# Kernel optimization log

Hardware: AMD Instinct MI355X
Metric: run time of the kernel (lower is better)

## Reference

```python
import jax, jax.numpy as jnp
import numpy as np

T, H, I, E, K = 1024, 1024, 512, 32, 4   # tokens, hidden, moe_inter, n_experts, top_k
G, TG, NS = 8, 4, 2                      # n_group, topk_group, n_shared_experts
C = 2 * T * K // E                       # expert capacity (no-drop headroom)
SCALE = 2.5                              # routed_scaling_factor


def setup_inputs() -> dict:
    key = jax.random.key(0)
    ks = jax.random.split(key, 7)
    s = 0.02
    return dict(
        hidden_states=jax.random.normal(ks[0], (T, H), jnp.float32),
        gate_w=jax.random.normal(ks[1], (E, H), jnp.float32) * s,
        e_bias=jax.random.normal(ks[2], (E,), jnp.float32) * 0.1,
        w_gate_up=jax.random.normal(ks[3], (E, 2 * I, H), jnp.float32) * s,
        w_down=jax.random.normal(ks[4], (E, H, I), jnp.float32) * s,
        w_gate_up_shared=jax.random.normal(ks[5], (2 * I * NS, H), jnp.float32) * s,
        w_down_shared=jax.random.normal(ks[6], (H, I * NS), jnp.float32) * s,
    )


def reference(hidden_states, gate_w, e_bias, w_gate_up, w_down, w_gate_up_shared, w_down_shared):
    x = hidden_states                                   # (T, H)
    # --- gate + sigmoid scoring (noaux_tc) ---
    logits = x @ gate_w.T                               # (T, E)
    scores = jax.nn.sigmoid(logits.astype(jnp.float32))
    sfc = scores + e_bias                               # scores_for_choice
    # --- group-limited top-k: top-2 sum per group, keep topk_group groups ---
    group_scores = jax.lax.top_k(sfc.reshape(T, G, E // G), 2)[0].sum(-1)  # (T, G)
    grp_idx = jax.lax.top_k(group_scores, TG)[1]        # (T, TG)
    gmask = jnp.zeros((T, G), jnp.float32).at[jnp.arange(T)[:, None], grp_idx].set(1.0)
    smask = jnp.repeat(gmask, E // G, axis=1)           # (T, E)
    sfc_m = jnp.where(smask > 0, sfc, 0.0)
    topk_idx = jax.lax.top_k(sfc_m, K)[1]               # (T, K)
    tw = jnp.take_along_axis(scores, topk_idx, axis=1)  # weights from raw scores
    tw = tw / (tw.sum(-1, keepdims=True) + 1e-20)       # norm_topk_prob
    tw = tw * SCALE
    # --- capacity-based dispatch (position within expert via cumsum of one-hot) ---
    e_flat = topk_idx.reshape(-1)                       # (T*K,)
    oh = jax.nn.one_hot(e_flat, E, dtype=jnp.float32)   # (T*K, E)
    pos = jnp.sum((jnp.cumsum(oh, axis=0) - 1.0) * oh, axis=-1).astype(jnp.int32)
    keep = (pos < C).astype(jnp.float32)                # capacity sized to never drop
    pos_c = jnp.clip(pos, 0, C - 1)
    t_flat = jnp.repeat(jnp.arange(T), K)
    combine = jnp.zeros((T, E, C), jnp.float32).at[t_flat, e_flat, pos_c].add(tw.reshape(-1) * keep)
    dispatch = jnp.zeros((T, E, C), jnp.float32).at[t_flat, e_flat, pos_c].add(keep)
    # --- grouped expert MLP (gate_up -> SiluAndMul -> down) ---
    xe = jnp.einsum('tec,th->ech', dispatch, x)         # (E, C, H)
    gu = jnp.einsum('ech,eoh->eco', xe, w_gate_up)      # (E, C, 2I)
    act = jax.nn.silu(gu[..., :I]) * gu[..., I:]
    ye = jnp.einsum('eci,ehi->ech', act, w_down)        # (E, C, H)
    routed = jnp.einsum('tec,ech->th', combine, ye)     # (T, H)
    # --- shared experts MLP on residual ---
    IS = I * NS
    gus = x @ w_gate_up_shared.T                        # (T, 2*IS)
    acts = jax.nn.silu(gus[:, :IS]) * gus[:, IS:]
    shared = acts @ w_down_shared.T                     # (T, H)
    return routed + shared
```

## Files before the change

kernel.cpp:

```cpp
#include <hip/hip_runtime.h>
#include <hip/hip_bf16.h>
#include <math.h>

#define T_TOK 1024
#define H_DIM 1024
#define I_DIM 512
#define E_NUM 32
#define K_TOP 4
#define G_NUM 8
#define TG_NUM 4
#define CAP 256
#define IS_DIM 1024
#define RSCALE 2.5f

#define MAXTILES 72

#define WS_CNT_OFF    0
#define WS_NT_OFF     128
#define WS_TILE_OFF   256
#define WS_EIDX_OFF   4096
#define WS_WN_OFF     20480
#define WS_STOK_OFF   36864
#define WS_SW_OFF     69632
#define WS_XB_OFF     102400
#define WS_ACT_OFF    (102400 + (size_t)T_TOK*H_DIM*2)
#define WS_ACTS_OFF   (WS_ACT_OFF + (size_t)E_NUM*CAP*I_DIM*2)

typedef __attribute__((ext_vector_type(8))) short short8v;
typedef __attribute__((ext_vector_type(4))) float f32x4;
typedef __attribute__((ext_vector_type(4))) unsigned uint4v;

__device__ __forceinline__ short f2bf(float f) {
    unsigned u = __float_as_uint(f);
    u += 0x7FFFu + ((u >> 16) & 1u);
    return (short)(u >> 16);
}
__device__ __forceinline__ unsigned pk2bf(float a, float b) {
    unsigned ua = __float_as_uint(a) + 0x8000u;
    unsigned ub = __float_as_uint(b) + 0x8000u;
    return __builtin_amdgcn_perm(ub, ua, 0x07060302);
}
__device__ __forceinline__ uint4v pk8bf(float4 lo, float4 hi) {
    uint4v r; r.x = pk2bf(lo.x, lo.y); r.y = pk2bf(lo.z, lo.w);
    r.z = pk2bf(hi.x, hi.y); r.w = pk2bf(hi.z, hi.w); return r;
}
__device__ __forceinline__ float silu_(float g) { return g / (1.f + expf(-g)); }

#define LDSTRIDE 40

__global__ __launch_bounds__(256) void xconv_kernel(const float* __restrict__ x,
                                                    short* __restrict__ xb) {
    const int i = (blockIdx.x * 256 + threadIdx.x) * 8;
    float4 a = *(const float4*)(x + i);
    float4 b = *(const float4*)(x + i + 4);
    *(uint4v*)(xb + i) = pk8bf(a, b);
}

__global__ __launch_bounds__(256) void gate_kernel(
    const float* __restrict__ x, const float* __restrict__ gate_w,
    const float* __restrict__ e_bias,
    int* __restrict__ eidx, float* __restrict__ wnorm)
{
    __shared__ float xs[H_DIM];
    __shared__ float logits[E_NUM];
    const int t = blockIdx.x;
    const int tid = threadIdx.x;
    ((float4*)xs)[tid] = ((const float4*)(x + (size_t)t * H_DIM))[tid];
    __syncthreads();

    const int e = tid >> 3, sub = tid & 7;
    const float4* gw4 = (const float4*)(gate_w + (size_t)e * H_DIM + sub * 128);
    const float4* xr4 = (const float4*)(xs + sub * 128);
    float p = 0.f;
    #pragma unroll
    for (int h = 0; h < 32; ++h) {
        float4 a = xr4[h], b = gw4[h];
        p += a.x * b.x + a.y * b.y + a.z * b.z + a.w * b.w;
    }
    for (int off = 4; off; off >>= 1) p += __shfl_down(p, off, 8);
    if (sub == 0) logits[e] = p;
    __syncthreads();
    if (tid != 0) return;

    float sc[E_NUM], sfc[E_NUM];
    for (int i = 0; i < E_NUM; ++i) {
        sc[i] = 1.f / (1.f + expf(-logits[i]));
        sfc[i] = sc[i] + e_bias[i];
    }
    float gs[G_NUM];
    for (int g = 0; g < G_NUM; ++g) {
        float m1 = -1e30f, m2 = -1e30f;
        for (int j = 0; j < E_NUM / G_NUM; ++j) {
            float v = sfc[g * (E_NUM / G_NUM) + j];
            if (v > m1) { m2 = m1; m1 = v; } else if (v > m2) m2 = v;
        }
        gs[g] = m1 + m2;
    }
    bool gm[G_NUM];
    for (int g = 0; g < G_NUM; ++g) gm[g] = false;
    for (int it = 0; it < TG_NUM; ++it) {
        int best = -1; float bv = -1e30f;
        for (int g = 0; g < G_NUM; ++g) if (!gm[g] && gs[g] > bv) { bv = gs[g]; best = g; }
        gm[best] = true;
    }
    float sm[E_NUM];
    for (int i = 0; i < E_NUM; ++i) sm[i] = gm[i / (E_NUM / G_NUM)] ? sfc[i] : 0.0f;
    int idx[K_TOP]; float w[K_TOP]; float tsum = 0.f;
    for (int it = 0; it < K_TOP; ++it) {
        int best = 0; float bv = -1e30f;
        for (int i = 0; i < E_NUM; ++i) if (sm[i] > bv) { bv = sm[i]; best = i; }
        sm[best] = -1e30f;
        idx[it] = best; w[it] = sc[best]; tsum += w[it];
    }
    float inv = RSCALE / (tsum + 1e-20f);
    const int base = t * K_TOP;
    for (int it = 0; it < K_TOP; ++it) {
        eidx[base + it] = idx[it];
        wnorm[base + it] = w[it] * inv;
    }
}

__global__ __launch_bounds__(256) void assign_kernel(
    const int* __restrict__ eidx, const float* __restrict__ wnorm,
    int* __restrict__ cnt, int* __restrict__ slot_token, float* __restrict__ slot_w,
    int* __restrict__ ntiles, int* __restrict__ tiles)
{
    __shared__ int   se[T_TOK * K_TOP];
    __shared__ float swt[T_TOK * K_TOP];
    __shared__ int   scnt[E_NUM];
    const int tid = threadIdx.x;
    for (int i = tid; i < T_TOK * K_TOP; i += 256) { se[i] = eidx[i]; swt[i] = wnorm[i]; }
    __syncthreads();

    const int e = tid >> 3;
    const int seg = tid & 7;
    const int base = seg * 512;
    int c = 0;
    for (int i = 0; i < 512; ++i) c += (se[base + i] == e);
    int excl = 0, total = 0;
    for (int s = 0; s < 8; ++s) {
        int cs = __shfl(c, s, 8);
        total += cs;
        if (s < seg) excl += cs;
    }
    if (seg == 0) { cnt[e] = total; scnt[e] = total; }
    int pos = excl;
    for (int i = 0; i < 512; ++i) {
        if (se[base + i] == e) {
            if (pos < CAP) {
                slot_token[e * CAP + pos] = (base + i) >> 2;
                slot_w[e * CAP + pos] = swt[base + i];
            }
            ++pos;
        }
    }
    __syncthreads();
    if (tid == 0) {
        int nt = 0;
        for (int t0 = 0; t0 < T_TOK; t0 += 128) {
            tiles[nt * 4] = -1; tiles[nt * 4 + 1] = t0; tiles[nt * 4 + 2] = 128; ++nt;
        }
        for (int ee = 0; ee < E_NUM; ++ee) {
            int n = min(scnt[ee], CAP);
            for (int r = 0; r < n; r += 128) {
                tiles[nt * 4] = ee; tiles[nt * 4 + 1] = r; tiles[nt * 4 + 2] = n; ++nt;
            }
        }
        *ntiles = nt;
    }
}

#define WAVE_SETUP() \
    const int tid = threadIdx.x; const int lane = tid & 63; const int wid = tid >> 6; \
    const int wm = wid & 1, wn = wid >> 1; \
    const int lr16 = lane & 15, kc = lane >> 4; \
    const int srow = tid >> 1, kh = (tid & 1) * 16;

#define DECL_ACC() f32x4 acc[4][4]; \
    _Pragma("unroll") for (int i_ = 0; i_ < 4; ++i_) \
    _Pragma("unroll") for (int j_ = 0; j_ < 4; ++j_) acc[i_][j_] = 0.f;

#define COMPUTE_4x4(Asb, Bsb) do { \
    short8v a_[4], b_[4]; \
    _Pragma("unroll") for (int mt = 0; mt < 4; ++mt) \
        a_[mt] = *(const short8v*)&(Asb)[(wm*64 + mt*16 + lr16)*LDSTRIDE + kc*8]; \
    _Pragma("unroll") for (int nt = 0; nt < 4; ++nt) \
        b_[nt] = *(const short8v*)&(Bsb)[(wn*64 + nt*16 + lr16)*LDSTRIDE + kc*8]; \
    _Pragma("unroll") for (int mt = 0; mt < 4; ++mt) \
    _Pragma("unroll") for (int nt = 0; nt < 4; ++nt) \
        acc[mt][nt] = __builtin_amdgcn_mfma_f32_16x16x32_bf16(a_[mt], b_[nt], acc[mt][nt], 0, 0, 0); \
} while (0)

__global__ __launch_bounds__(256, 3) void gu_all_kernel(
    const short* __restrict__ xb, const float* __restrict__ w_gate_up,
    const float* __restrict__ w_gus,
    const int* __restrict__ ntiles, const int* __restrict__ tiles,
    const int* __restrict__ slot_token, const float* __restrict__ slot_w,
    short* __restrict__ act, short* __restrict__ acts)
{
    if ((int)blockIdx.y >= *ntiles) return;
    const int e  = tiles[blockIdx.y * 4];
    const int r0 = tiles[blockIdx.y * 4 + 1];
    const int ne = tiles[blockIdx.y * 4 + 2];
    const bool sh = (e < 0);
    if (!sh && blockIdx.x >= I_DIM / 64) return;
    const int col0 = blockIdx.x * 64;

    __shared__ __align__(16) short As[2][128 * LDSTRIDE];
    __shared__ __align__(16) short Bs[2][128 * LDSTRIDE];
    __shared__ int   toks[128];
    __shared__ float sws[128];

    WAVE_SETUP();
    if (tid < 128) {
        if (sh) { toks[tid] = r0 + tid; sws[tid] = 1.f; }
        else {
            int p = r0 + tid; bool v = p < ne;
            toks[tid] = v ? slot_token[e * CAP + p] : 0;
            sws[tid]  = v ? slot_w[e * CAP + p] : 0.f;
        }
    }
    __syncthreads();

    const int IDim = sh ? IS_DIM : I_DIM;
    const float* wbase = sh ? w_gus : (w_gate_up + (size_t)e * (2 * I_DIM) * H_DIM);
    const int c = srow;
    const int wr = ((c >> 4) & 1) * IDim + col0 + ((c >> 5) << 4) + (c & 15);
    const short* aptr = xb + (size_t)toks[srow] * H_DIM + kh;
    const float* bptr = wbase + (size_t)wr * H_DIM + kh;
    const int off = srow * LDSTRIDE + kh;

    DECL_ACC();
    short8v cA0 = *(const short8v*)(aptr), cA1 = *(const short8v*)(aptr + 8);
    float4 cB0 = *(const float4*)(bptr),     cB1 = *(const float4*)(bptr + 4);
    float4 cB2 = *(const float4*)(bptr + 8), cB3 = *(const float4*)(bptr + 12);

    int buf = 0;
    for (int k0 = 0; k0 < H_DIM; k0 += 32) {
        short8v nA0, nA1; float4 nB0, nB1, nB2, nB3;
        const int k1 = k0 + 32;
        if (k1 < H_DIM) {
            nA0 = *(const short8v*)(aptr + k1); nA1 = *(const short8v*)(aptr + k1 + 8);
            nB0 = *(const float4*)(bptr + k1);     nB1 = *(const float4*)(bptr + k1 + 4);
            nB2 = *(const float4*)(bptr + k1 + 8); nB3 = *(const float4*)(bptr + k1 + 12);
        }
        *(short8v*)&As[buf][off]     = cA0;
        *(short8v*)&As[buf][off + 8] = cA1;
        *(uint4v*)&Bs[buf][off]      = pk8bf(cB0, cB1);
        *(uint4v*)&Bs[buf][off + 8]  = pk8bf(cB2, cB3);
        __syncthreads();
        COMPUTE_4x4(As[buf], Bs[buf]);
        buf ^= 1;
        cA0 = nA0; cA1 = nA1; cB0 = nB0; cB1 = nB1; cB2 = nB2; cB3 = nB3;
    }

    short* rowbase = sh ? (acts + (size_t)r0 * IS_DIM)
                        : (act + ((size_t)e * CAP + r0) * I_DIM);
    const int nmax = sh ? 128 : (ne - r0);
    #pragma unroll
    for (int mt = 0; mt < 4; ++mt) {
        #pragma unroll
        for (int q = 0; q < 2; ++q) {
            f32x4 g = acc[mt][2 * q], u = acc[mt][2 * q + 1];
            int colI = col0 + wn * 32 + q * 16 + lr16;
            #pragma unroll
            for (int i = 0; i < 4; ++i) {
                int rl = wm * 64 + mt * 16 + kc * 4 + i;
                if (rl < nmax) {
                    float s = sws[rl];
                    rowbase[(size_t)rl * IDim + colI] = f2bf(s * silu_(g[i]) * u[i]);
                }
            }
        }
    }
}

__global__ __launch_bounds__(256, 3) void down_all_kernel(
    const short* __restrict__ act, const short* __restrict__ acts,
    const float* __restrict__ w_down, const float* __restrict__ w_ds,
    const int* __restrict__ ntiles, const int* __restrict__ tiles,
    const int* __restrict__ slot_token, float* __restrict__ out)
{
    if ((int)blockIdx.y >= *ntiles) return;
    const int e  = tiles[blockIdx.y * 4];
    const int r0 = tiles[blockIdx.y * 4 + 1];
    const int ne = tiles[blockIdx.y * 4 + 2];
    const bool sh = (e < 0);
    const int h0 = blockIdx.x * 128;

    __shared__ __align__(16) short As[2][128 * LDSTRIDE];
    __shared__ __align__(16) short Bs[2][128 * LDSTRIDE];
    __shared__ int toks[128];

    WAVE_SETUP();
    if (tid < 128) {
        if (sh) toks[tid] = r0 + tid;
        else {
            int p = r0 + tid;
            toks[tid] = (p < ne) ? slot_token[e * CAP + p] : 0;
        }
    }
    __syncthreads();

    const int Kdim = sh ? IS_DIM : I_DIM;
    const short* aptr = (sh ? (acts + (size_t)(r0 + srow) * IS_DIM)
                            : (act + ((size_t)e * CAP + r0 + srow) * I_DIM)) + kh;
    const float* bptr = (sh ? w_ds : (w_down + (size_t)e * H_DIM * I_DIM))
                        + (size_t)(h0 + srow) * Kdim + kh;
    const int off = srow * LDSTRIDE + kh;

    DECL_ACC();
    short8v cA0 = *(const short8v*)(aptr), cA1 = *(const short8v*)(aptr + 8);
    float4 cB0 = *(const float4*)(bptr),     cB1 = *(const float4*)(bptr + 4);
    float4 cB2 = *(const float4*)(bptr + 8), cB3 = *(const float4*)(bptr + 12);

    int buf = 0;
    for (int k0 = 0; k0 < Kdim; k0 += 32) {
        short8v nA0, nA1; float4 nB0, nB1, nB2, nB3;
        const int k1 = k0 + 32;
        if (k1 < Kdim) {
            nA0 = *(const short8v*)(aptr + k1); nA1 = *(const short8v*)(aptr + k1 + 8);
            nB0 = *(const float4*)(bptr + k1);     nB1 = *(const float4*)(bptr + k1 + 4);
            nB2 = *(const float4*)(bptr + k1 + 8); nB3 = *(const float4*)(bptr + k1 + 12);
        }
        *(short8v*)&As[buf][off]     = cA0;
        *(short8v*)&As[buf][off + 8] = cA1;
        *(uint4v*)&Bs[buf][off]      = pk8bf(cB0, cB1);
        *(uint4v*)&Bs[buf][off + 8]  = pk8bf(cB2, cB3);
        __syncthreads();
        COMPUTE_4x4(As[buf], Bs[buf]);
        buf ^= 1;
        cA0 = nA0; cA1 = nA1; cB0 = nB0; cB1 = nB1; cB2 = nB2; cB3 = nB3;
    }

    const int nmax = sh ? 128 : (ne - r0);
    #pragma unroll
    for (int mt = 0; mt < 4; ++mt) {
        #pragma unroll
        for (int i = 0; i < 4; ++i) {
            int rl = wm * 64 + mt * 16 + kc * 4 + i;
            if (rl < nmax) {
                float* orow = out + (size_t)toks[rl] * H_DIM + h0 + wn * 64;
                #pragma unroll
                for (int nt = 0; nt < 4; ++nt)
                    atomicAdd(&orow[nt * 16 + lr16], acc[mt][nt][i]);
            }
        }
    }
}

extern "C" void kernel_launch(void* const* d_in, const int* in_sizes, int n_in,
                              void* d_out, int out_size, void* d_ws, size_t ws_size,
                              hipStream_t stream) {
    const float* x   = (const float*)d_in[0];
    const float* gw  = (const float*)d_in[1];
    const float* eb  = (const float*)d_in[2];
    const float* wgu = (const float*)d_in[3];
    const float* wd  = (const float*)d_in[4];
    const float* wgs = (const float*)d_in[5];
    const float* wds = (const float*)d_in[6];
    float* out = (float*)d_out;
    char* ws = (char*)d_ws;

    int*   cnt    = (int*)(ws + WS_CNT_OFF);
    int*   ntiles = (int*)(ws + WS_NT_OFF);
    int*   tiles  = (int*)(ws + WS_TILE_OFF);
    int*   eidx   = (int*)(ws + WS_EIDX_OFF);
    float* wnorm  = (float*)(ws + WS_WN_OFF);
    int*   stok   = (int*)(ws + WS_STOK_OFF);
    float* sw     = (float*)(ws + WS_SW_OFF);
    short* xb     = (short*)(ws + WS_XB_OFF);
    short* act    = (short*)(ws + WS_ACT_OFF);
    short* acts   = (short*)(ws + WS_ACTS_OFF);

    hipMemsetAsync(out, 0, (size_t)T_TOK * H_DIM * sizeof(float), stream);
    xconv_kernel<<<T_TOK * H_DIM / (256 * 8), 256, 0, stream>>>(x, xb);
    gate_kernel<<<T_TOK, 256, 0, stream>>>(x, gw, eb, eidx, wnorm);
    assign_kernel<<<1, 256, 0, stream>>>(eidx, wnorm, cnt, stok, sw, ntiles, tiles);
    gu_all_kernel<<<dim3(IS_DIM / 64, MAXTILES), 256, 0, stream>>>(
        xb, wgu, wgs, ntiles, tiles, stok, sw, act, acts);
    down_all_kernel<<<dim3(H_DIM / 128, MAXTILES), 256, 0, stream>>>(
        act, acts, wd, wds, ntiles, tiles, stok, out);
}
```

Before: 429.6 us.

## Fuse bf16 conversion into gate kernel and switch GEMMs to single-buffered BK=64 tiles

Removes the separate xconv kernel by writing the bf16 copy of x from the gate kernel, which already loads each row. Both grouped GEMM kernels move from a register-prefetched double-buffered K=32 loop to a single-buffered K=64 loop with a padded LDS stride of 76, halving the number of barrier pairs per K. It also drops the occupancy hint of 3 blocks per CU from launch bounds. In exchange, global loads are no longer prefetched ahead of compute, so latency hiding depends on other resident waves.

```diff
diff --git a/kernel.cpp b/kernel.cpp
--- a/kernel.cpp
+++ b/kernel.cpp
@@ -29,6 +29,7 @@
 typedef __attribute__((ext_vector_type(8))) short short8v;
 typedef __attribute__((ext_vector_type(4))) float f32x4;
 typedef __attribute__((ext_vector_type(4))) unsigned uint4v;
+typedef __attribute__((ext_vector_type(2))) unsigned uint2v;
 
 __device__ __forceinline__ short f2bf(float f) {
     unsigned u = __float_as_uint(f);
@@ -46,26 +47,21 @@
 }
 __device__ __forceinline__ float silu_(float g) { return g / (1.f + expf(-g)); }
 
-#define LDSTRIDE 40
-
-__global__ __launch_bounds__(256) void xconv_kernel(const float* __restrict__ x,
-                                                    short* __restrict__ xb) {
-    const int i = (blockIdx.x * 256 + threadIdx.x) * 8;
-    float4 a = *(const float4*)(x + i);
-    float4 b = *(const float4*)(x + i + 4);
-    *(uint4v*)(xb + i) = pk8bf(a, b);
-}
+#define LDST 76
 
 __global__ __launch_bounds__(256) void gate_kernel(
     const float* __restrict__ x, const float* __restrict__ gate_w,
     const float* __restrict__ e_bias,
-    int* __restrict__ eidx, float* __restrict__ wnorm)
+    int* __restrict__ eidx, float* __restrict__ wnorm, short* __restrict__ xb)
 {
     __shared__ float xs[H_DIM];
     __shared__ float logits[E_NUM];
     const int t = blockIdx.x;
     const int tid = threadIdx.x;
-    ((float4*)xs)[tid] = ((const float4*)(x + (size_t)t * H_DIM))[tid];
+    float4 xv = ((const float4*)(x + (size_t)t * H_DIM))[tid];
+    ((float4*)xs)[tid] = xv;
+    uint2v xp; xp.x = pk2bf(xv.x, xv.y); xp.y = pk2bf(xv.z, xv.w);
+    *(uint2v*)(xb + (size_t)t * H_DIM + tid * 4) = xp;
     __syncthreads();
 
     const int e = tid >> 3, sub = tid & 7;
@@ -174,24 +170,26 @@
     const int tid = threadIdx.x; const int lane = tid & 63; const int wid = tid >> 6; \
     const int wm = wid & 1, wn = wid >> 1; \
     const int lr16 = lane & 15, kc = lane >> 4; \
-    const int srow = tid >> 1, kh = (tid & 1) * 16;
+    const int sr = tid >> 1, skh = (tid & 1) * 32;
 
 #define DECL_ACC() f32x4 acc[4][4]; \
     _Pragma("unroll") for (int i_ = 0; i_ < 4; ++i_) \
     _Pragma("unroll") for (int j_ = 0; j_ < 4; ++j_) acc[i_][j_] = 0.f;
 
-#define COMPUTE_4x4(Asb, Bsb) do { \
-    short8v a_[4], b_[4]; \
-    _Pragma("unroll") for (int mt = 0; mt < 4; ++mt) \
-        a_[mt] = *(const short8v*)&(Asb)[(wm*64 + mt*16 + lr16)*LDSTRIDE + kc*8]; \
-    _Pragma("unroll") for (int nt = 0; nt < 4; ++nt) \
-        b_[nt] = *(const short8v*)&(Bsb)[(wn*64 + nt*16 + lr16)*LDSTRIDE + kc*8]; \
-    _Pragma("unroll") for (int mt = 0; mt < 4; ++mt) \
-    _Pragma("unroll") for (int nt = 0; nt < 4; ++nt) \
-        acc[mt][nt] = __builtin_amdgcn_mfma_f32_16x16x32_bf16(a_[mt], b_[nt], acc[mt][nt], 0, 0, 0); \
+#define COMPUTE_BK64(Asb, Bsb) do { \
+    _Pragma("unroll") for (int s_ = 0; s_ < 2; ++s_) { \
+        short8v a_[4], b_[4]; \
+        _Pragma("unroll") for (int mt = 0; mt < 4; ++mt) \
+            a_[mt] = *(const short8v*)&(Asb)[(wm*64 + mt*16 + lr16)*LDST + s_*32 + kc*8]; \
+        _Pragma("unroll") for (int nt = 0; nt < 4; ++nt) \
+            b_[nt] = *(const short8v*)&(Bsb)[(wn*64 + nt*16 + lr16)*LDST + s_*32 + kc*8]; \
+        _Pragma("unroll") for (int mt = 0; mt < 4; ++mt) \
+        _Pragma("unroll") for (int nt = 0; nt < 4; ++nt) \
+            acc[mt][nt] = __builtin_amdgcn_mfma_f32_16x16x32_bf16(a_[mt], b_[nt], acc[mt][nt], 0, 0, 0); \
+    } \
 } while (0)
 
-__global__ __launch_bounds__(256, 3) void gu_all_kernel(
+__global__ __launch_bounds__(256) void gu_all_kernel(
     const short* __restrict__ xb, const float* __restrict__ w_gate_up,
     const float* __restrict__ w_gus,
     const int* __restrict__ ntiles, const int* __restrict__ tiles,
@@ -206,8 +204,8 @@
     if (!sh && blockIdx.x >= I_DIM / 64) return;
     const int col0 = blockIdx.x * 64;
 
-    __shared__ __align__(16) short As[2][128 * LDSTRIDE];
-    __shared__ __align__(16) short Bs[2][128 * LDSTRIDE];
+    __shared__ __align__(16) short As[128 * LDST];
+    __shared__ __align__(16) short Bs[128 * LDST];
     __shared__ int   toks[128];
     __shared__ float sws[128];
 
@@ -224,34 +222,37 @@
 
     const int IDim = sh ? IS_DIM : I_DIM;
     const float* wbase = sh ? w_gus : (w_gate_up + (size_t)e * (2 * I_DIM) * H_DIM);
-    const int c = srow;
+    const int c = sr;
     const int wr = ((c >> 4) & 1) * IDim + col0 + ((c >> 5) << 4) + (c & 15);
-    const short* aptr = xb + (size_t)toks[srow] * H_DIM + kh;
-    const float* bptr = wbase + (size_t)wr * H_DIM + kh;
-    const int off = srow * LDSTRIDE + kh;
+    const short* aptr = xb + (size_t)toks[sr] * H_DIM + skh;
+    const float* bptr = wbase + (size_t)wr * H_DIM + skh;
+    const int off = sr * LDST + skh;
 
     DECL_ACC();
-    short8v cA0 = *(const short8v*)(aptr), cA1 = *(const short8v*)(aptr + 8);
-    float4 cB0 = *(const float4*)(bptr),     cB1 = *(const float4*)(bptr + 4);
-    float4 cB2 = *(const float4*)(bptr + 8), cB3 = *(const float4*)(bptr + 12);
-
-    int buf = 0;
-    for (int k0 = 0; k0 < H_DIM; k0 += 32) {
-        short8v nA0, nA1; float4 nB0, nB1, nB2, nB3;
-        const int k1 = k0 + 32;
-        if (k1 < H_DIM) {
-            nA0 = *(const short8v*)(aptr + k1); nA1 = *(const short8v*)(aptr + k1 + 8);
-            nB0 = *(const float4*)(bptr + k1);     nB1 = *(const float4*)(bptr + k1 + 4);
-            nB2 = *(const float4*)(bptr + k1 + 8); nB3 = *(const float4*)(bptr + k1 + 12);
-        }
-        *(short8v*)&As[buf][off]     = cA0;
-        *(short8v*)&As[buf][off + 8] = cA1;
-        *(uint4v*)&Bs[buf][off]      = pk8bf(cB0, cB1);
-        *(uint4v*)&Bs[buf][off + 8]  = pk8bf(cB2, cB3);
+    for (int k0 = 0; k0 < H_DIM; k0 += 64) {
+        short8v a0 = *(const short8v*)(aptr + k0);
+        short8v a1 = *(const short8v*)(aptr + k0 + 8);
+        short8v a2 = *(const short8v*)(aptr + k0 + 16);
+        short8v a3 = *(const short8v*)(aptr + k0 + 24);
+        float4 b0 = *(const float4*)(bptr + k0);
+        float4 b1 = *(const float4*)(bptr + k0 + 4);
+        float4 b2 = *(const float4*)(bptr + k0 + 8);
+        float4 b3 = *(const float4*)(bptr + k0 + 12);
+        float4 b4 = *(const float4*)(bptr + k0 + 16);
+        float4 b5 = *(const float4*)(bptr + k0 + 20);
+        float4 b6 = *(const float4*)(bptr + k0 + 24);
+        float4 b7 = *(const float4*)(bptr + k0 + 28);
         __syncthreads();
-        COMPUTE_4x4(As[buf], Bs[buf]);
-        buf ^= 1;
-        cA0 = nA0; cA1 = nA1; cB0 = nB0; cB1 = nB1; cB2 = nB2; cB3 = nB3;
+        *(short8v*)&As[off]      = a0;
+        *(short8v*)&As[off + 8]  = a1;
+        *(short8v*)&As[off + 16] = a2;
+        *(short8v*)&As[off + 24] = a3;
+        *(uint4v*)&Bs[off]       = pk8bf(b0, b1);
+        *(uint4v*)&Bs[off + 8]   = pk8bf(b2, b3);
+        *(uint4v*)&Bs[off + 16]  = pk8bf(b4, b5);
+        *(uint4v*)&Bs[off + 24]  = pk8bf(b6, b7);
+        __syncthreads();
+        COMPUTE_BK64(As, Bs);
     }
 
     short* rowbase = sh ? (acts + (size_t)r0 * IS_DIM)
@@ -275,7 +276,7 @@
     }
 }
 
-__global__ __launch_bounds__(256, 3) void down_all_kernel(
+__global__ __launch_bounds__(256) void down_all_kernel(
     const short* __restrict__ act, const short* __restrict__ acts,
     const float* __restrict__ w_down, const float* __restrict__ w_ds,
     const int* __restrict__ ntiles, const int* __restrict__ tiles,
@@ -288,8 +289,8 @@
     const bool sh = (e < 0);
     const int h0 = blockIdx.x * 128;
 
-    __shared__ __align__(16) short As[2][128 * LDSTRIDE];
-    __shared__ __align__(16) short Bs[2][128 * LDSTRIDE];
+    __shared__ __align__(16) short As[128 * LDST];
+    __shared__ __align__(16) short Bs[128 * LDST];
     __shared__ int toks[128];
 
     WAVE_SETUP();
@@ -303,34 +304,37 @@
     __syncthreads();
 
     const int Kdim = sh ? IS_DIM : I_DIM;
-    const short* aptr = (sh ? (acts + (size_t)(r0 + srow) * IS_DIM)
-                            : (act + ((size_t)e * CAP + r0 + srow) * I_DIM)) + kh;
+    const short* aptr = (sh ? (acts + (size_t)(r0 + sr) * IS_DIM)
+                            : (act + ((size_t)e * CAP + r0 + sr) * I_DIM)) + skh;
     const float* bptr = (sh ? w_ds : (w_down + (size_t)e * H_DIM * I_DIM))
-                        + (size_t)(h0 + srow) * Kdim + kh;
-    const int off = srow * LDSTRIDE + kh;
+                        + (size_t)(h0 + sr) * Kdim + skh;
+    const int off = sr * LDST + skh;
 
     DECL_ACC();
-    short8v cA0 = *(const short8v*)(aptr), cA1 = *(const short8v*)(aptr + 8);
-    float4 cB0 = *(const float4*)(bptr),     cB1 = *(const float4*)(bptr + 4);
-    float4 cB2 = *(const float4*)(bptr + 8), cB3 = *(const float4*)(bptr + 12);
-
-    int buf = 0;
-    for (int k0 = 0; k0 < Kdim; k0 += 32) {
-        short8v nA0, nA1; float4 nB0, nB1, nB2, nB3;
-        const int k1 = k0 + 32;
-        if (k1 < Kdim) {
-            nA0 = *(const short8v*)(aptr + k1); nA1 = *(const short8v*)(aptr + k1 + 8);
-            nB0 = *(const float4*)(bptr + k1);     nB1 = *(const float4*)(bptr + k1 + 4);
-            nB2 = *(const float4*)(bptr + k1 + 8); nB3 = *(const float4*)(bptr + k1 + 12);
-        }
-        *(short8v*)&As[buf][off]     = cA0;
-        *(short8v*)&As[buf][off + 8] = cA1;
-        *(uint4v*)&Bs[buf][off]      = pk8bf(cB0, cB1);
-        *(uint4v*)&Bs[buf][off + 8]  = pk8bf(cB2, cB3);
+    for (int k0 = 0; k0 < Kdim; k0 += 64) {
+        short8v a0 = *(const short8v*)(aptr + k0);
+        short8v a1 = *(const short8v*)(aptr + k0 + 8);
+        short8v a2 = *(const short8v*)(aptr + k0 + 16);
+        short8v a3 = *(const short8v*)(aptr + k0 + 24);
+        float4 b0 = *(const float4*)(bptr + k0);
+        float4 b1 = *(const float4*)(bptr + k0 + 4);
+        float4 b2 = *(const float4*)(bptr + k0 + 8);
+        float4 b3 = *(const float4*)(bptr + k0 + 12);
+        float4 b4 = *(const float4*)(bptr + k0 + 16);
+        float4 b5 = *(const float4*)(bptr + k0 + 20);
+        float4 b6 = *(const float4*)(bptr + k0 + 24);
+        float4 b7 = *(const float4*)(bptr + k0 + 28);
         __syncthreads();
-        COMPUTE_4x4(As[buf], Bs[buf]);
-        buf ^= 1;
-        cA0 = nA0; cA1 = nA1; cB0 = nB0; cB1 = nB1; cB2 = nB2; cB3 = nB3;
+        *(short8v*)&As[off]      = a0;
+        *(short8v*)&As[off + 8]  = a1;
+        *(short8v*)&As[off + 16] = a2;
+        *(short8v*)&As[off + 24] = a3;
+        *(uint4v*)&Bs[off]       = pk8bf(b0, b1);
+        *(uint4v*)&Bs[off + 8]   = pk8bf(b2, b3);
+        *(uint4v*)&Bs[off + 16]  = pk8bf(b4, b5);
+        *(uint4v*)&Bs[off + 24]  = pk8bf(b6, b7);
+        __syncthreads();
+        COMPUTE_BK64(As, Bs);
     }
 
     const int nmax = sh ? 128 : (ne - r0);
@@ -374,8 +378,7 @@
     short* acts   = (short*)(ws + WS_ACTS_OFF);
 
     hipMemsetAsync(out, 0, (size_t)T_TOK * H_DIM * sizeof(float), stream);
-    xconv_kernel<<<T_TOK * H_DIM / (256 * 8), 256, 0, stream>>>(x, xb);
-    gate_kernel<<<T_TOK, 256, 0, stream>>>(x, gw, eb, eidx, wnorm);
+    gate_kernel<<<T_TOK, 256, 0, stream>>>(x, gw, eb, eidx, wnorm, xb);
     assign_kernel<<<1, 256, 0, stream>>>(eidx, wnorm, cnt, stok, sw, ntiles, tiles);
     gu_all_kernel<<<dim3(IS_DIM / 64, MAXTILES), 256, 0, stream>>>(
         xb, wgu, wgs, ntiles, tiles, stok, sw, act, acts);
```

After: 440.6 us. 2.6% more time.
